# Performance work log

Hardware: AMD Instinct MI355X
Metric: run time of the kernel (lower is better)

The kernel has to match this reference:

```python
import jax, jax.numpy as jnp
import numpy as np

ALPHA = 0.2  # LeakyReLU negative slope


def setup_inputs() -> dict:
    key = jax.random.key(0)
    k1, k2, k3, k4 = jax.random.split(key, 4)
    B, N, Fin, Fout = 8, 2048, 256, 256
    h = jax.random.normal(k1, (B, N, Fin), dtype=jnp.float32)
    # random 0/1 adjacency with guaranteed self-loops so every row has a neighbor
    adj = jax.random.randint(k2, (N, N), 0, 2).astype(jnp.float32)
    adj = jnp.maximum(adj, jnp.eye(N, dtype=jnp.float32))
    # xavier_uniform with gain=1.414
    def xavier(k, shape, gain=1.414):
        fan_in, fan_out = shape[0], shape[1]
        a = gain * np.sqrt(6.0 / (fan_in + fan_out))
        return jax.random.uniform(k, shape, dtype=jnp.float32, minval=-a, maxval=a)
    W = xavier(k3, (Fin, Fout))
    a = xavier(k4, (2 * Fout, 1))
    return {"h": h, "adj_matrix": adj, "W": W, "a": a}


def reference(h, adj_matrix, W, a):
    # h: [B, N, Fin], adj_matrix: [N, N], W: [Fin, Fout], a: [2*Fout, 1]
    Fout = W.shape[1]
    Wh = jnp.einsum("bnf,fo->bno", h, W)            # [B, N, Fout]
    a1, a2 = a[:Fout, 0], a[Fout:, 0]                 # split additive attention vector
    # e[b,i,j] = leakyrelu(Wh[b,i]@a1 + Wh[b,j]@a2) — equals concat([Wh_i,Wh_j])@a
    s1 = Wh @ a1                                      # [B, N]
    s2 = Wh @ a2                                      # [B, N]
    e = s1[:, :, None] + s2[:, None, :]               # [B, N, N]
    e = jnp.where(e >= 0, e, ALPHA * e)               # LeakyReLU
    e = jnp.where(adj_matrix[None] == 0, -jnp.inf, e)  # mask non-edges
    attention = jax.nn.softmax(e, axis=-1)            # [B, N, N]
    # dropout is identity in eval mode (training=False)
    h_prime = jnp.einsum("bij,bjo->bio", attention, Wh)
    return h_prime
```

## Files before the change

kernel.cpp:

```cpp
#include <hip/hip_runtime.h>
#include <cstdint>

#define NN 2048
#define LOG2E 1.4426950408889634f

typedef __attribute__((ext_vector_type(8))) short bf16x8;
typedef __attribute__((ext_vector_type(4))) float f32x4;

__device__ __forceinline__ unsigned short f2bf(float x){
  union { float f; unsigned u; } v; v.f = x;
  unsigned r = v.u + 0x7FFFu + ((v.u >> 16) & 1u);
  return (unsigned short)(r >> 16);
}
__device__ __forceinline__ unsigned pack2(float a, float b){
  return (unsigned)f2bf(a) | ((unsigned)f2bf(b) << 16);
}
__device__ __forceinline__ unsigned permpack(unsigned hi, unsigned lo){
  return __builtin_amdgcn_perm(hi, lo, 0x07060302u);
}

__global__ __launch_bounds__(256) void k_prep(const float* __restrict__ adj,
                                              const float* __restrict__ W,
                                              unsigned long long* __restrict__ ab,
                                              unsigned short* __restrict__ Wt){
  int tid = threadIdx.x;
  if (blockIdx.x < 2048){
    int i = blockIdx.x;
    int w = tid >> 6, lane = tid & 63;
    #pragma unroll
    for (int seg = 0; seg < 8; seg++){
      int j = seg * 256 + tid;
      unsigned long long m = __ballot(adj[(size_t)i * NN + j] != 0.0f);
      if (lane == 0) ab[i * 32 + seg * 4 + w] = m;
    }
  } else {
    int g = (blockIdx.x - 2048) * 256 + tid;
    int o = g >> 8, k = g & 255;
    Wt[g] = f2bf(W[k * 256 + o]);
  }
}

__global__ __launch_bounds__(512, 2) void k_fused_gemm(const float* __restrict__ h,
                                                       const unsigned short* __restrict__ Wt,
                                                       const float* __restrict__ a,
                                                       unsigned short* __restrict__ WhT,
                                                       float* __restrict__ s1c,
                                                       float* __restrict__ s2c){
  __shared__ __align__(16) unsigned char As[2 * 8192];
  __shared__ __align__(16) unsigned short Ts[256 * 72];
  __shared__ float s1p[8][64], s2p[8][64];
  const int tid = threadIdx.x;
  const int r0 = blockIdx.x * 64;
  const int b  = r0 >> 11;
  const int i0 = r0 & (NN - 1);
  const int w = tid >> 6, lane = tid & 63, lhi = lane >> 4, llo = lane & 15;
  const int wc = w * 32;
  const int sit = w >> 1, skk = w & 1;
  const int srow = sit * 16 + llo;
  const int skol = skk * 32 + lhi * 8;

  f32x4 acc[4][2];
  #pragma unroll
  for (int i = 0; i < 4; i++)
    #pragma unroll
    for (int j = 0; j < 2; j++){ acc[i][j][0]=0.f; acc[i][j][1]=0.f; acc[i][j][2]=0.f; acc[i][j][3]=0.f; }

  float4 hv[4][2];
  #pragma unroll
  for (int t = 0; t < 4; t++){
    const float* hp = h + (size_t)(r0 + srow) * 256 + t * 64 + skol;
    hv[t][0] = *(const float4*)hp;
    hv[t][1] = *(const float4*)(hp + 4);
  }

  auto loadB = [&](int k0, bf16x8* dst){
    #pragma unroll
    for (int ot = 0; ot < 2; ot++)
      #pragma unroll
      for (int kk = 0; kk < 2; kk++)
        dst[ot * 2 + kk] = *(const bf16x8*)(Wt + (size_t)(wc + ot * 16 + llo) * 256 + k0 + kk * 32 + lhi * 8);
  };
  bf16x8 bfr[2][4];
  loadB(0, bfr[0]);

  #pragma unroll
  for (int t = 0; t < 4; t++){
    uint4 q = make_uint4(pack2(hv[t][0].x, hv[t][0].y), pack2(hv[t][0].z, hv[t][0].w),
                         pack2(hv[t][1].x, hv[t][1].y), pack2(hv[t][1].z, hv[t][1].w));
    *(uint4*)&As[(t & 1) * 8192 + w * 1024 + lane * 16] = q;
    __syncthreads();
    if (t < 3) loadB((t + 1) * 64, bfr[(t + 1) & 1]);
    bf16x8 af[2][4];
    #pragma unroll
    for (int kk = 0; kk < 2; kk++)
      #pragma unroll
      for (int it = 0; it < 4; it++)
        af[kk][it] = *(const bf16x8*)&As[(t & 1) * 8192 + (it * 2 + kk) * 1024 + lane * 16];
    #pragma unroll
    for (int kk = 0; kk < 2; kk++)
      #pragma unroll
      for (int it = 0; it < 4; it++)
        #pragma unroll
        for (int ot = 0; ot < 2; ot++)
          acc[it][ot] = __builtin_amdgcn_mfma_f32_16x16x32_bf16(af[kk][it], bfr[t & 1][ot * 2 + kk], acc[it][ot], 0, 0, 0);
  }

  float a1v[2], a2v[2];
  #pragma unroll
  for (int ot = 0; ot < 2; ot++){
    a1v[ot] = a[wc + ot * 16 + llo] * LOG2E;
    a2v[ot] = a[256 + wc + ot * 16 + llo] * LOG2E;
  }
  #pragma unroll
  for (int it = 0; it < 4; it++){
    #pragma unroll
    for (int q = 0; q < 4; q++){
      float p1 = acc[it][0][q] * a1v[0] + acc[it][1][q] * a1v[1];
      float p2 = acc[it][0][q] * a2v[0] + acc[it][1][q] * a2v[1];
      #pragma unroll
      for (int o = 1; o < 16; o <<= 1){ p1 += __shfl_xor(p1, o); p2 += __shfl_xor(p2, o); }
      if (llo == 0){
        s1p[w][it * 16 + lhi * 4 + q] = p1;
        s2p[w][it * 16 + lhi * 4 + q] = p2;
      }
    }
  }

  #pragma unroll
  for (int it = 0; it < 4; it++){
    #pragma unroll
    for (int ot = 0; ot < 2; ot++){
      int o = wc + ot * 16 + llo;
      uint2 u = make_uint2(pack2(acc[it][ot][0], acc[it][ot][1]),
                           pack2(acc[it][ot][2], acc[it][ot][3]));
      *(uint2*)&Ts[o * 72 + it * 16 + lhi * 4] = u;
    }
  }
  __syncthreads();

  if (tid < 64){
    float t1 = 0.f, t2 = 0.f;
    #pragma unroll
    for (int g = 0; g < 8; g++){ t1 += s1p[g][tid]; t2 += s2p[g][tid]; }
    s1c[r0 + tid] = t1;
    s2c[r0 + tid] = t2;
  }
  #pragma unroll
  for (int p = 0; p < 4; p++){
    int o = p * 64 + (tid >> 3), col = (tid & 7) * 8;
    *(uint4*)(WhT + (size_t)(b * 256 + o) * 2048 + i0 + col) = *(const uint4*)&Ts[o * 72 + col];
  }
}

__global__ __launch_bounds__(512, 2) void k_attn(const float* __restrict__ s1c,
                                                 const float* __restrict__ s2c,
                                                 const unsigned short* __restrict__ WhT,
                                                 const unsigned long long* __restrict__ ab,
                                                 float* __restrict__ out){
  __shared__ __align__(16) float s2s[2048];
  __shared__ __align__(16) unsigned char PsB[2 * 8192];
  __shared__ __align__(16) unsigned char bitsB[64 * 264];
  __shared__ float s1s[64], lin[64], red[8], rsp[8][64];
  const int tid = threadIdx.x;
  const int bid = blockIdx.x;
  const int b = bid & 7, i0 = (bid >> 3) * 64;
  const int w = tid >> 6, lane = tid & 63, lhi = lane >> 4, llo = lane & 15;
  const int wc = w * 32;
  const int sit = w >> 1, skk = w & 1;
  const int prow = sit * 16 + llo;

  float4 v = ((const float4*)(s2c + (size_t)b * NN))[tid];
  ((float4*)s2s)[tid] = v;
  float vmax = fmaxf(fmaxf(v.x, v.y), fmaxf(v.z, v.w));
  #pragma unroll
  for (int o = 32; o; o >>= 1) vmax = fmaxf(vmax, __shfl_xor(vmax, o));
  if (lane == 0) red[w] = vmax;
  if (tid < 64) s1s[tid] = s1c[(size_t)b * NN + i0 + tid];
  #pragma unroll
  for (int k = 0; k < 4; k++){
    int g = k * 512 + tid;
    unsigned long long mw = ab[(size_t)i0 * 32 + g];
    *(unsigned long long*)&bitsB[(g >> 5) * 264 + (g & 31) * 8] = mw;
  }
  __syncthreads();
  float m2 = red[0];
  #pragma unroll
  for (int g = 1; g < 8; g++) m2 = fmaxf(m2, red[g]);

  const float s1v = s1s[prow];
  const float xm = s1v + m2;
  const float mv = fmaxf(xm, 0.2f * xm);
  const float c1 = s1v - mv;
  const float c2 = 0.2f * s1v - mv;
  float rs = 0.f;

  f32x4 acc[4][2];
  #pragma unroll
  for (int i = 0; i < 4; i++)
    #pragma unroll
    for (int j = 0; j < 2; j++){ acc[i][j][0]=0.f; acc[i][j][1]=0.f; acc[i][j][2]=0.f; acc[i][j][3]=0.f; }

  auto loadB = [&](int j0, bf16x8* dst){
    #pragma unroll
    for (int ot = 0; ot < 2; ot++)
      #pragma unroll
      for (int kk = 0; kk < 2; kk++)
        dst[ot * 2 + kk] = *(const bf16x8*)(WhT + (size_t)(b * 256 + wc + ot * 16 + llo) * 2048 + j0 + kk * 32 + lhi * 8);
  };

  unsigned puq[4];
  auto computeP = [&](int tn){
    unsigned bits = bitsB[prow * 264 + tn * 8 + skk * 4 + lhi];
    const float* sp = &s2s[tn * 64 + skk * 32 + lhi * 8];
    float4 xa = *(const float4*)sp;
    float4 xb = *(const float4*)(sp + 4);
    float xs[8] = {xa.x, xa.y, xa.z, xa.w, xb.x, xb.y, xb.z, xb.w};
    unsigned pu[8];
    #pragma unroll
    for (int e = 0; e < 8; e++){
      float s2v = xs[e];
      float y = fmaxf(s2v + c1, __builtin_fmaf(0.2f, s2v, c2));
      float p = __builtin_amdgcn_exp2f(y);
      unsigned m = ((bits >> e) & 1u) ? 0xFFFF0000u : 0u;
      unsigned u = __float_as_uint(p) & m;
      rs += __uint_as_float(u);
      pu[e] = u;
    }
    puq[0] = permpack(pu[1], pu[0]); puq[1] = permpack(pu[3], pu[2]);
    puq[2] = permpack(pu[5], pu[4]); puq[3] = permpack(pu[7], pu[6]);
  };

  auto stageBody = [&](int t, int BUF, bf16x8* curB, bf16x8* nxtB, bool last){
    *(uint4*)&PsB[BUF * 8192 + w * 1024 + lane * 16] = *(uint4*)&puq[0];
    __syncthreads();
    if (!last) loadB((t + 1) * 64, nxtB);
    bf16x8 af[2][4];
    #pragma unroll
    for (int kk = 0; kk < 2; kk++)
      #pragma unroll
      for (int it = 0; it < 4; it++)
        af[kk][it] = *(const bf16x8*)&PsB[BUF * 8192 + (it * 2 + kk) * 1024 + lane * 16];
    if (!last) computeP(t + 1);
    #pragma unroll
    for (int kk = 0; kk < 2; kk++)
      #pragma unroll
      for (int it = 0; it < 4; it++)
        #pragma unroll
        for (int ot = 0; ot < 2; ot++)
          acc[it][ot] = __builtin_amdgcn_mfma_f32_16x16x32_bf16(af[kk][it], curB[ot * 2 + kk], acc[it][ot], 0, 0, 0);
  };

  bf16x8 bA[4], bB[4];
  loadB(0, bA);
  computeP(0);
  for (int t2 = 0; t2 < 32; t2 += 2){
    stageBody(t2,     0, bA, bB, false);
    stageBody(t2 + 1, 1, bB, bA, t2 + 1 == 31);
  }

  rs += __shfl_xor(rs, 16);
  rs += __shfl_xor(rs, 32);
  if (lhi == 0) rsp[w][prow] = rs;
  __syncthreads();
  if (tid < 64){
    int it = tid >> 4;
    lin[tid] = 1.0f / (rsp[it * 2][tid] + rsp[it * 2 + 1][tid]);
  }
  __syncthreads();

  #pragma unroll
  for (int it = 0; it < 4; it++){
    #pragma unroll
    for (int ot = 0; ot < 2; ot++){
      int col = wc + ot * 16 + llo;
      #pragma unroll
      for (int q = 0; q < 4; q++){
        int row = it * 16 + lhi * 4 + q;
        out[(size_t)(b * NN + i0 + row) * 256 + col] = acc[it][ot][q] * lin[row];
      }
    }
  }
}

extern "C" void kernel_launch(void* const* d_in, const int* in_sizes, int n_in,
                              void* d_out, int out_size, void* d_ws, size_t ws_size,
                              hipStream_t stream) {
  const float* h   = (const float*)d_in[0];
  const float* adj = (const float*)d_in[1];
  const float* W   = (const float*)d_in[2];
  const float* a   = (const float*)d_in[3];
  float* out = (float*)d_out;

  char* ws = (char*)d_ws;
  unsigned short* WhT      = (unsigned short*)(ws);
  unsigned short* Wt       = (unsigned short*)(ws + 8388608);
  unsigned long long* ab   = (unsigned long long*)(ws + 8519680);
  float* s1c               = (float*)(ws + 9043968);
  float* s2c               = (float*)(ws + 9109504);

  hipLaunchKernelGGL(k_prep,       dim3(2304), dim3(256), 0, stream, adj, W, ab, Wt);
  hipLaunchKernelGGL(k_fused_gemm, dim3(256),  dim3(512), 0, stream, h, Wt, a, WhT, s1c, s2c);
  hipLaunchKernelGGL(k_attn,       dim3(256),  dim3(512), 0, stream, s1c, s2c, WhT, ab, out);
}
```

Baseline: 134.4 us.

## Compute attention probabilities in registers per warp, dropping LDS P exchange and barriers

The attention kernel now splits warps 2x4 over rows and output columns, so each warp computes its own P fragments directly in MFMA A-operand layout. This removes the shared-memory P staging buffer and the per-tile __syncthreads. The cost is redundant exp computation: each row's probabilities are recomputed by the four warps sharing it, and B fragments double to 8 registers per stage. The GEMM kernel's block-to-(batch,row) mapping is also interleaved by batch to match the attention kernel's order.

```diff
diff --git a/kernel.cpp b/kernel.cpp
--- a/kernel.cpp
+++ b/kernel.cpp
@@ -50,9 +50,10 @@
   __shared__ __align__(16) unsigned short Ts[256 * 72];
   __shared__ float s1p[8][64], s2p[8][64];
   const int tid = threadIdx.x;
-  const int r0 = blockIdx.x * 64;
-  const int b  = r0 >> 11;
-  const int i0 = r0 & (NN - 1);
+  const int bid = blockIdx.x;
+  const int b  = bid & 7;
+  const int i0 = (bid >> 3) * 64;
+  const size_t r0 = (size_t)b * NN + i0;
   const int w = tid >> 6, lane = tid & 63, lhi = lane >> 4, llo = lane & 15;
   const int wc = w * 32;
   const int sit = w >> 1, skk = w & 1;
@@ -68,7 +69,7 @@
   float4 hv[4][2];
   #pragma unroll
   for (int t = 0; t < 4; t++){
-    const float* hp = h + (size_t)(r0 + srow) * 256 + t * 64 + skol;
+    const float* hp = h + (r0 + srow) * 256 + t * 64 + skol;
     hv[t][0] = *(const float4*)hp;
     hv[t][1] = *(const float4*)(hp + 4);
   }
@@ -152,22 +153,20 @@
   }
 }
 
-__global__ __launch_bounds__(512, 2) void k_attn(const float* __restrict__ s1c,
-                                                 const float* __restrict__ s2c,
-                                                 const unsigned short* __restrict__ WhT,
-                                                 const unsigned long long* __restrict__ ab,
-                                                 float* __restrict__ out){
+__global__ __launch_bounds__(512) void k_attn(const float* __restrict__ s1c,
+                                              const float* __restrict__ s2c,
+                                              const unsigned short* __restrict__ WhT,
+                                              const unsigned long long* __restrict__ ab,
+                                              float* __restrict__ out){
   __shared__ __align__(16) float s2s[2048];
-  __shared__ __align__(16) unsigned char PsB[2 * 8192];
   __shared__ __align__(16) unsigned char bitsB[64 * 264];
-  __shared__ float s1s[64], lin[64], red[8], rsp[8][64];
+  __shared__ float s1s[64], red[8];
   const int tid = threadIdx.x;
   const int bid = blockIdx.x;
   const int b = bid & 7, i0 = (bid >> 3) * 64;
   const int w = tid >> 6, lane = tid & 63, lhi = lane >> 4, llo = lane & 15;
-  const int wc = w * 32;
-  const int sit = w >> 1, skk = w & 1;
-  const int prow = sit * 16 + llo;
+  const int wi = w & 1, wo = w >> 1;
+  const int co = wo * 64;
 
   float4 v = ((const float4*)(s2c + (size_t)b * NN))[tid];
   ((float4*)s2s)[tid] = v;
@@ -187,97 +186,95 @@
   #pragma unroll
   for (int g = 1; g < 8; g++) m2 = fmaxf(m2, red[g]);
 
-  const float s1v = s1s[prow];
-  const float xm = s1v + m2;
-  const float mv = fmaxf(xm, 0.2f * xm);
-  const float c1 = s1v - mv;
-  const float c2 = 0.2f * s1v - mv;
-  float rs = 0.f;
-
-  f32x4 acc[4][2];
-  #pragma unroll
-  for (int i = 0; i < 4; i++)
-    #pragma unroll
-    for (int j = 0; j < 2; j++){ acc[i][j][0]=0.f; acc[i][j][1]=0.f; acc[i][j][2]=0.f; acc[i][j][3]=0.f; }
-
-  auto loadB = [&](int j0, bf16x8* dst){
-    #pragma unroll
-    for (int ot = 0; ot < 2; ot++)
+  float c1[2], c2[2], rs[2];
+  #pragma unroll
+  for (int it = 0; it < 2; it++){
+    float s1v = s1s[wi * 32 + it * 16 + llo];
+    float xm = s1v + m2;
+    float mv = fmaxf(xm, 0.2f * xm);
+    c1[it] = s1v - mv;
+    c2[it] = 0.2f * s1v - mv;
+    rs[it] = 0.f;
+  }
+
+  f32x4 acc[2][4];
+  #pragma unroll
+  for (int i = 0; i < 2; i++)
+    #pragma unroll
+    for (int j = 0; j < 4; j++){ acc[i][j][0]=0.f; acc[i][j][1]=0.f; acc[i][j][2]=0.f; acc[i][j][3]=0.f; }
+
+  auto loadB = [&](int t, bf16x8* dst){
+    #pragma unroll
+    for (int ot = 0; ot < 4; ot++)
       #pragma unroll
       for (int kk = 0; kk < 2; kk++)
-        dst[ot * 2 + kk] = *(const bf16x8*)(WhT + (size_t)(b * 256 + wc + ot * 16 + llo) * 2048 + j0 + kk * 32 + lhi * 8);
+        dst[ot * 2 + kk] = *(const bf16x8*)(WhT + (size_t)(b * 256 + co + ot * 16 + llo) * 2048 + t * 64 + kk * 32 + lhi * 8);
   };
 
-  unsigned puq[4];
-  auto computeP = [&](int tn){
-    unsigned bits = bitsB[prow * 264 + tn * 8 + skk * 4 + lhi];
-    const float* sp = &s2s[tn * 64 + skk * 32 + lhi * 8];
-    float4 xa = *(const float4*)sp;
-    float4 xb = *(const float4*)(sp + 4);
-    float xs[8] = {xa.x, xa.y, xa.z, xa.w, xb.x, xb.y, xb.z, xb.w};
-    unsigned pu[8];
-    #pragma unroll
-    for (int e = 0; e < 8; e++){
-      float s2v = xs[e];
-      float y = fmaxf(s2v + c1, __builtin_fmaf(0.2f, s2v, c2));
-      float p = __builtin_amdgcn_exp2f(y);
-      unsigned m = ((bits >> e) & 1u) ? 0xFFFF0000u : 0u;
-      unsigned u = __float_as_uint(p) & m;
-      rs += __uint_as_float(u);
-      pu[e] = u;
-    }
-    puq[0] = permpack(pu[1], pu[0]); puq[1] = permpack(pu[3], pu[2]);
-    puq[2] = permpack(pu[5], pu[4]); puq[3] = permpack(pu[7], pu[6]);
+  auto computeP = [&](int t, bf16x8* af){
+    #pragma unroll
+    for (int it = 0; it < 2; it++){
+      #pragma unroll
+      for (int kk = 0; kk < 2; kk++){
+        unsigned bits = bitsB[(wi * 32 + it * 16 + llo) * 264 + t * 8 + kk * 4 + lhi];
+        const float* sp = &s2s[t * 64 + kk * 32 + lhi * 8];
+        float4 xa = *(const float4*)sp;
+        float4 xb = *(const float4*)(sp + 4);
+        float xs[8] = {xa.x, xa.y, xa.z, xa.w, xb.x, xb.y, xb.z, xb.w};
+        unsigned pu[8];
+        #pragma unroll
+        for (int e = 0; e < 8; e++){
+          float s2v = xs[e];
+          float y = fmaxf(s2v + c1[it], __builtin_fmaf(0.2f, s2v, c2[it]));
+          float p = __builtin_amdgcn_exp2f(y);
+          unsigned m = ((bits >> e) & 1u) ? 0xFFFF0000u : 0u;
+          unsigned u = __float_as_uint(p) & m;
+          rs[it] += __uint_as_float(u);
+          pu[e] = u;
+        }
+        uint4 q = make_uint4(permpack(pu[1], pu[0]), permpack(pu[3], pu[2]),
+                             permpack(pu[5], pu[4]), permpack(pu[7], pu[6]));
+        af[it * 2 + kk] = *(bf16x8*)&q;
+      }
+    }
   };
 
-  auto stageBody = [&](int t, int BUF, bf16x8* curB, bf16x8* nxtB, bool last){
-    *(uint4*)&PsB[BUF * 8192 + w * 1024 + lane * 16] = *(uint4*)&puq[0];
-    __syncthreads();
-    if (!last) loadB((t + 1) * 64, nxtB);
-    bf16x8 af[2][4];
+  auto doMFMA = [&](bf16x8* af, bf16x8* bf){
     #pragma unroll
     for (int kk = 0; kk < 2; kk++)
       #pragma unroll
-      for (int it = 0; it < 4; it++)
-        af[kk][it] = *(const bf16x8*)&PsB[BUF * 8192 + (it * 2 + kk) * 1024 + lane * 16];
-    if (!last) computeP(t + 1);
-    #pragma unroll
-    for (int kk = 0; kk < 2; kk++)
-      #pragma unroll
-      for (int it = 0; it < 4; it++)
+      for (int it = 0; it < 2; it++)
         #pragma unroll
-        for (int ot = 0; ot < 2; ot++)
-          acc[it][ot] = __builtin_amdgcn_mfma_f32_16x16x32_bf16(af[kk][it], curB[ot * 2 + kk], acc[it][ot], 0, 0, 0);
+        for (int ot = 0; ot < 4; ot++)
+          acc[it][ot] = __builtin_amdgcn_mfma_f32_16x16x32_bf16(af[it * 2 + kk], bf[ot * 2 + kk], acc[it][ot], 0, 0, 0);
   };
 
-  bf16x8 bA[4], bB[4];
-  loadB(0, bA);
-  computeP(0);
-  for (int t2 = 0; t2 < 32; t2 += 2){
-    stageBody(t2,     0, bA, bB, false);
-    stageBody(t2 + 1, 1, bB, bA, t2 + 1 == 31);
-  }
-
-  rs += __shfl_xor(rs, 16);
-  rs += __shfl_xor(rs, 32);
-  if (lhi == 0) rsp[w][prow] = rs;
-  __syncthreads();
-  if (tid < 64){
-    int it = tid >> 4;
-    lin[tid] = 1.0f / (rsp[it * 2][tid] + rsp[it * 2 + 1][tid]);
-  }
-  __syncthreads();
-
-  #pragma unroll
-  for (int it = 0; it < 4; it++){
-    #pragma unroll
-    for (int ot = 0; ot < 2; ot++){
-      int col = wc + ot * 16 + llo;
-      #pragma unroll
-      for (int q = 0; q < 4; q++){
-        int row = it * 16 + lhi * 4 + q;
-        out[(size_t)(b * NN + i0 + row) * 256 + col] = acc[it][ot][q] * lin[row];
-      }
+  bf16x8 b0[8], b1[8], af0[4], af1[4];
+  loadB(0, b0);
+  computeP(0, af0);
+  for (int t = 0; t < 32; t += 2){
+    loadB(t + 1, b1);
+    computeP(t + 1, af1);
+    doMFMA(af0, b0);
+    if (t + 2 < 32){ loadB(t + 2, b0); computeP(t + 2, af0); }
+    doMFMA(af1, b1);
+  }
+
+  #pragma unroll
+  for (int it = 0; it < 2; it++){
+    rs[it] += __shfl_xor(rs[it], 16);
+    rs[it] += __shfl_xor(rs[it], 32);
+  }
+  #pragma unroll
+  for (int it = 0; it < 2; it++){
+    float lv = 1.0f / rs[it];
+    #pragma unroll
+    for (int q = 0; q < 4; q++){
+      float l = __shfl(lv, lhi * 4 + q);
+      int row = i0 + wi * 32 + it * 16 + lhi * 4 + q;
+      #pragma unroll
+      for (int ot = 0; ot < 4; ot++)
+        out[(size_t)(b * NN + row) * 256 + co + ot * 16 + llo] = acc[it][ot][q] * l;
     }
   }
 }
```

New measurement: 157.5 us. +17.2%, slower.
